# Kernel tuning notes

Measured on AMD Instinct MI355X. Metric: run time of the kernel, lower is better.

## Reference

```python
import jax, jax.numpy as jnp
import numpy as np

FEATURES = 1024
HEAD_DIM = 64
NUM_HEADS = 16
EPS = 1e-5


def setup_inputs() -> dict:
    key = jax.random.key(0)
    ks = jax.random.split(key, 6)
    x = jax.random.normal(ks[0], (2, 2048, FEATURES), dtype=jnp.float32)
    s_in = 1.0 / np.sqrt(FEATURES)
    s_hd = 1.0 / np.sqrt(NUM_HEADS * HEAD_DIM)
    return {
        "x": x,
        "gamma": jnp.ones((FEATURES,), jnp.float32),
        "beta": jnp.zeros((FEATURES,), jnp.float32),
        "Wq": jax.random.normal(ks[1], (FEATURES, NUM_HEADS * HEAD_DIM), jnp.float32) * s_in,
        "Wkv": jax.random.normal(ks[2], (FEATURES, 2 * HEAD_DIM), jnp.float32) * s_in,
        "Wo": jax.random.normal(ks[3], (NUM_HEADS * HEAD_DIM, FEATURES), jnp.float32) * s_hd,
        "bo": jax.random.normal(ks[4], (FEATURES,), jnp.float32) * s_hd,
    }


def reference(x, gamma, beta, Wq, Wkv, Wo, bo):
    # LayerNorm over last dim
    mu = jnp.mean(x, axis=-1, keepdims=True)
    var = jnp.mean(jnp.square(x - mu), axis=-1, keepdims=True)
    xn = (x - mu) * jax.lax.rsqrt(var + EPS) * gamma + beta

    b, t, _ = x.shape
    q = (xn @ Wq).reshape(b, t, NUM_HEADS, HEAD_DIM).transpose(0, 2, 1, 3)  # b h t d
    kv = xn @ Wkv  # b s 2d
    k, v = kv[..., :HEAD_DIM], kv[..., HEAD_DIM:]  # b s d (single shared head)

    scale = HEAD_DIM ** (-0.5)
    attn = jnp.einsum('bhtd,bsd->bhts', q, k) * scale
    attn = jax.nn.softmax(attn, axis=-1)
    out = jnp.einsum('bhts,bsd->bhtd', attn, v)
    out = out.transpose(0, 2, 1, 3).reshape(b, t, NUM_HEADS * HEAD_DIM)
    return out @ Wo + bo + x
```

## Files before the change

kernel.cpp:

```cpp
#include <hip/hip_runtime.h>

typedef __attribute__((ext_vector_type(8))) __bf16 bf16x8;
typedef __attribute__((ext_vector_type(4))) float floatx4;
typedef unsigned short u16;
typedef unsigned int u32;

#define KSCALE 0.18033688011112042f

__device__ __forceinline__ u16 f2bf(float f) {
    union { float f; u32 u; } v; v.f = f;
    u32 r = v.u + 0x7fffu + ((v.u >> 16) & 1u);
    return (u16)(r >> 16);
}

__device__ __forceinline__ u32 pk2bf(float a, float b) {
    union { float f; u32 u; } x, y; x.f = a; y.f = b;
    return __builtin_amdgcn_perm(y.u + 0x8000u, x.u + 0x8000u, 0x07060302);
}

__device__ __forceinline__ void gl_lds16(const u16* g, u16* l) {
    __builtin_amdgcn_global_load_lds((const __attribute__((address_space(1))) void*)g,
                                     (__attribute__((address_space(3))) void*)l, 16, 0, 0);
}

__global__ __launch_bounds__(256) void prep(const float* __restrict__ Wq, const float* __restrict__ Wkv,
                                            const float* __restrict__ Wo, const float* __restrict__ x,
                                            const float* __restrict__ gamma, const float* __restrict__ beta,
                                            u16* __restrict__ WqkvT, u16* __restrict__ WoT,
                                            u16* __restrict__ xn) {
    __shared__ float tile[64][68];
    __shared__ float ps[4], ps2[4];
    const int bx = blockIdx.x;
    const int t = threadIdx.x;
    if (bx < 768) {
        const int z = bx >> 8, rem = bx & 255;
        const int tr = (rem >> 4) * 64, tc = (rem & 15) * 64;
        const float* in = (z == 0) ? Wq : (z == 1 ? Wkv : Wo);
        u16* out = (z == 0) ? WqkvT : (z == 1 ? WqkvT + (size_t)1024 * 1024 : WoT);
        const int cols = (z == 1) ? 128 : 1024;
        if (tc >= cols) return;
        for (int p = 0; p < 4; p++) {
            int ri = (t >> 4) + p * 16;
            int ci = (t & 15) * 4;
            float4 v = *(const float4*)&in[(size_t)(tr + ri) * cols + tc + ci];
            tile[ri][ci + 0] = v.x; tile[ri][ci + 1] = v.y;
            tile[ri][ci + 2] = v.z; tile[ri][ci + 3] = v.w;
        }
        __syncthreads();
        for (int p = 0; p < 4; p++) {
            int oc = (t >> 4) + p * 16;
            int ir = (t & 15) * 4;
            float s = (z == 1 && (tc + oc) < 64) ? KSCALE : 1.0f;
            ushort4 o;
            o.x = f2bf(tile[ir + 0][oc] * s);
            o.y = f2bf(tile[ir + 1][oc] * s);
            o.z = f2bf(tile[ir + 2][oc] * s);
            o.w = f2bf(tile[ir + 3][oc] * s);
            *(ushort4*)&out[(size_t)(tc + oc) * 1024 + tr + ir] = o;
        }
    } else {
        const int row = bx - 768;
        const float* xr = x + (size_t)row * 1024;
        float4 v = *(const float4*)&xr[t * 4];
        float s = v.x + v.y + v.z + v.w;
        float s2 = v.x * v.x + v.y * v.y + v.z * v.z + v.w * v.w;
        for (int off = 1; off < 64; off <<= 1) {
            s += __shfl_xor(s, off, 64);
            s2 += __shfl_xor(s2, off, 64);
        }
        int w = t >> 6, lane = t & 63;
        if (lane == 0) { ps[w] = s; ps2[w] = s2; }
        __syncthreads();
        float S = ps[0] + ps[1] + ps[2] + ps[3];
        float S2 = ps2[0] + ps2[1] + ps2[2] + ps2[3];
        float mu = S * (1.0f / 1024.0f);
        float var = S2 * (1.0f / 1024.0f) - mu * mu;
        float rstd = rsqrtf(var + 1e-5f);
        ushort4 o;
        o.x = f2bf((v.x - mu) * rstd * gamma[t * 4 + 0] + beta[t * 4 + 0]);
        o.y = f2bf((v.y - mu) * rstd * gamma[t * 4 + 1] + beta[t * 4 + 1]);
        o.z = f2bf((v.z - mu) * rstd * gamma[t * 4 + 2] + beta[t * 4 + 2]);
        o.w = f2bf((v.w - mu) * rstd * gamma[t * 4 + 3] + beta[t * 4 + 3]);
        *(ushort4*)&xn[(size_t)row * 1024 + t * 4] = o;
    }
}

template <bool FINAL>
__global__ __launch_bounds__(256) void gemm_bt(const u16* __restrict__ A, const u16* __restrict__ BT,
                                               u16* __restrict__ Cb, float* __restrict__ Cf,
                                               const float* __restrict__ bias, const float* __restrict__ resid,
                                               u16* __restrict__ vt2, int M, int N, int K) {
    __shared__ u16 as_[2 * 64 * 64];
    __shared__ u16 bs_[2 * 128 * 64];
    const int t = threadIdx.x;
    const int w = t >> 6, lane = t & 63, q = lane >> 4, c = lane & 15;
    const int tm = blockIdx.y * 64, tn = blockIdx.x * 128;
    const int wm = (w & 1) * 32, wn = (w >> 1) * 64;

    const int l3 = lane >> 3, sch = lane & 7;
    const int arow = w * 16 + l3;
    const int aswz = (sch ^ (arow & 7)) * 8;
    const int brow = w * 32 + l3;
    const int bswz = (sch ^ (brow & 7)) * 8;
    const u16* ag0 = A + (size_t)(tm + arow) * K + aswz;
    const u16* ag1 = ag0 + (size_t)8 * K;
    const u16* bg0 = BT + (size_t)(tn + brow) * K + bswz;
    const u16* bg1 = bg0 + (size_t)8 * K;
    const u16* bg2 = bg0 + (size_t)16 * K;
    const u16* bg3 = bg0 + (size_t)24 * K;
    u16* al0 = as_ + (w * 16) * 64;
    u16* al1 = as_ + (w * 16 + 8) * 64;
    u16* bl0 = bs_ + (w * 32) * 64;
    u16* bl1 = bs_ + (w * 32 + 8) * 64;
    u16* bl2 = bs_ + (w * 32 + 16) * 64;
    u16* bl3 = bs_ + (w * 32 + 24) * 64;

    const int c7 = c & 7;
    const u16* afp[2][2];
    const u16* bfp[4][2];
#pragma unroll
    for (int i = 0; i < 2; i++)
#pragma unroll
        for (int kk = 0; kk < 2; kk++)
            afp[i][kk] = &as_[(wm + i * 16 + c) * 64 + (((kk * 4 + q) ^ c7) * 8)];
#pragma unroll
    for (int j = 0; j < 4; j++)
#pragma unroll
        for (int kk = 0; kk < 2; kk++)
            bfp[j][kk] = &bs_[(wn + j * 16 + c) * 64 + (((kk * 4 + q) ^ c7) * 8)];

    floatx4 acc[2][4];
    for (int i = 0; i < 2; i++)
        for (int j = 0; j < 4; j++) acc[i][j] = (floatx4){0.f, 0.f, 0.f, 0.f};

    gl_lds16(ag0, al0);
    gl_lds16(ag1, al1);
    gl_lds16(bg0, bl0);
    gl_lds16(bg1, bl1);
    gl_lds16(bg2, bl2);
    gl_lds16(bg3, bl3);
    __syncthreads();

    const int NIT = K >> 6;
#pragma unroll 2
    for (int it = 0; it < NIT; it++) {
        const int cur = it & 1, nxt = cur ^ 1;
        if (it + 1 < NIT) {
            const int k0 = (it + 1) << 6;
            gl_lds16(ag0 + k0, al0 + nxt * 4096);
            gl_lds16(ag1 + k0, al1 + nxt * 4096);
            gl_lds16(bg0 + k0, bl0 + nxt * 8192);
            gl_lds16(bg1 + k0, bl1 + nxt * 8192);
            gl_lds16(bg2 + k0, bl2 + nxt * 8192);
            gl_lds16(bg3 + k0, bl3 + nxt * 8192);
        }
        bf16x8 af[2][2], bf[4][2];
#pragma unroll
        for (int i = 0; i < 2; i++)
#pragma unroll
            for (int kk = 0; kk < 2; kk++)
                af[i][kk] = *(const bf16x8*)(afp[i][kk] + cur * 4096);
#pragma unroll
        for (int j = 0; j < 4; j++)
#pragma unroll
            for (int kk = 0; kk < 2; kk++)
                bf[j][kk] = *(const bf16x8*)(bfp[j][kk] + cur * 8192);
#pragma unroll
        for (int kk = 0; kk < 2; kk++)
#pragma unroll
            for (int i = 0; i < 2; i++)
#pragma unroll
                for (int j = 0; j < 4; j++)
                    acc[i][j] = __builtin_amdgcn_mfma_f32_16x16x32_bf16(af[i][kk], bf[j][kk], acc[i][j], 0, 0, 0);
        __syncthreads();
    }
#pragma unroll
    for (int i = 0; i < 2; i++)
#pragma unroll
        for (int j = 0; j < 4; j++)
#pragma unroll
            for (int r = 0; r < 4; r++) {
                int row = tm + wm + i * 16 + q * 4 + r;
                int col = tn + wn + j * 16 + c;
                float v = acc[i][j][r];
                if (FINAL) {
                    Cf[(size_t)row * N + col] = v + bias[col] + resid[(size_t)row * N + col];
                } else if (col < 1088) {
                    Cb[(size_t)row * N + col] = f2bf(v);
                } else {
                    int d = col - 1088;
                    int bb = row >> 11, sl = row & 2047;
                    int Bk = sl >> 5, u = sl & 31;
                    int up = ((u >> 2) & 3) * 8 + ((u >> 4) << 2) + (u & 3);
                    vt2[((size_t)(bb * 64 + d)) * 2048 + Bk * 32 + up] = f2bf(v);
                }
            }
}

union Vf { bf16x8 v; u32 w[4]; };

__global__ __launch_bounds__(256, 2) void attn9(const u16* __restrict__ qkv, const u16* __restrict__ vt2,
                                                u16* __restrict__ out) {
    __shared__ u16 ksm[2][64 * 64];
    __shared__ u16 vsm[2][64 * 64];
    const int t = threadIdx.x;
    const int w = t >> 6, lane = t & 63;
    const int q = lane >> 4, c = lane & 15;
    const int qt = blockIdx.x, hg = blockIdx.y, b = blockIdx.z;
    const int h = hg * 4 + w;
    const size_t qrow0 = (size_t)b * 2048 + qt * 32;
    const u16* kbase = qkv + (size_t)b * 2048 * 1152 + 1024;
    const u16* vbase = vt2 + (size_t)b * 64 * 2048;

    const int l3 = lane >> 3, sch = lane & 7;
    const int srow = w * 16 + l3;
    const int swz = (sch ^ (srow & 7)) * 8;
    const u16* kg0 = kbase + (size_t)srow * 1152 + swz;
    const u16* kg1 = kg0 + (size_t)8 * 1152;
    const u16* vg0 = vbase + (size_t)srow * 2048 + swz;
    const u16* vg1 = vg0 + (size_t)8 * 2048;
    u16* kl0 = &ksm[0][(w * 16) * 64];
    u16* kl1 = &ksm[0][(w * 16 + 8) * 64];
    u16* vl0 = &vsm[0][(w * 16) * 64];
    u16* vl1 = &vsm[0][(w * 16 + 8) * 64];

    const int c7 = c & 7;
    const u16* kfp[4][2];
    const u16* vfp[4][2];
#pragma unroll
    for (int ni = 0; ni < 4; ni++)
#pragma unroll
        for (int kk = 0; kk < 2; kk++) {
            kfp[ni][kk] = &ksm[0][(ni * 16 + c) * 64 + (((kk * 4 + q) ^ c7) * 8)];
            vfp[ni][kk] = &vsm[0][(ni * 16 + c) * 64 + (((kk * 4 + q) ^ c7) * 8)];
        }

    bf16x8 qf[2][2];
#pragma unroll
    for (int mi = 0; mi < 2; mi++)
#pragma unroll
        for (int kk = 0; kk < 2; kk++)
            qf[mi][kk] = *(const bf16x8*)&qkv[(qrow0 + mi * 16 + c) * 1152 + h * 64 + kk * 32 + q * 8];

    floatx4 O[4][2], Lacc[2];
#pragma unroll
    for (int di = 0; di < 4; di++)
#pragma unroll
        for (int mi = 0; mi < 2; mi++) O[di][mi] = (floatx4){0.f, 0.f, 0.f, 0.f};
    Lacc[0] = (floatx4){0.f, 0.f, 0.f, 0.f};
    Lacc[1] = (floatx4){0.f, 0.f, 0.f, 0.f};
    Vf ones;
    ones.w[0] = ones.w[1] = ones.w[2] = ones.w[3] = 0x3F803F80u;

    gl_lds16(kg0, kl0);
    gl_lds16(kg1, kl1);
    gl_lds16(vg0, vl0);
    gl_lds16(vg1, vl1);
    kg0 += (size_t)64 * 1152; kg1 += (size_t)64 * 1152; vg0 += 64; vg1 += 64;
    __syncthreads();

#pragma unroll 2
    for (int tt = 0; tt < 32; tt++) {
        const int cur = tt & 1, nxt = cur ^ 1;
        if (tt < 31) {
            gl_lds16(kg0, kl0 + nxt * 4096);
            gl_lds16(kg1, kl1 + nxt * 4096);
            gl_lds16(vg0, vl0 + nxt * 4096);
            gl_lds16(vg1, vl1 + nxt * 4096);
            kg0 += (size_t)64 * 1152; kg1 += (size_t)64 * 1152; vg0 += 64; vg1 += 64;
        }

        bf16x8 kf[4][2];
        Vf vf[4][2];
#pragma unroll
        for (int ni = 0; ni < 4; ni++)
#pragma unroll
            for (int kk = 0; kk < 2; kk++)
                kf[ni][kk] = *(const bf16x8*)(kfp[ni][kk] + cur * 4096);
#pragma unroll
        for (int di = 0; di < 4; di++)
#pragma unroll
            for (int kk = 0; kk < 2; kk++)
                vf[di][kk].v = *(const bf16x8*)(vfp[di][kk] + cur * 4096);

        floatx4 sacc[4][2];
#pragma unroll
        for (int ni = 0; ni < 4; ni++)
#pragma unroll
            for (int mi = 0; mi < 2; mi++) {
                floatx4 z = (floatx4){0.f, 0.f, 0.f, 0.f};
                z = __builtin_amdgcn_mfma_f32_16x16x32_bf16(kf[ni][0], qf[mi][0], z, 0, 0, 0);
                z = __builtin_amdgcn_mfma_f32_16x16x32_bf16(kf[ni][1], qf[mi][1], z, 0, 0, 0);
                sacc[ni][mi] = z;
            }

        u32 pk[4][2][2];
#pragma unroll
        for (int mi = 0; mi < 2; mi++)
#pragma unroll
            for (int ni = 0; ni < 4; ni++) {
                float p0 = __builtin_amdgcn_exp2f(sacc[ni][mi][0]);
                float p1 = __builtin_amdgcn_exp2f(sacc[ni][mi][1]);
                float p2 = __builtin_amdgcn_exp2f(sacc[ni][mi][2]);
                float p3 = __builtin_amdgcn_exp2f(sacc[ni][mi][3]);
                pk[ni][mi][0] = pk2bf(p0, p1);
                pk[ni][mi][1] = pk2bf(p2, p3);
            }

#pragma unroll
        for (int kk = 0; kk < 2; kk++) {
            Vf pf[2];
#pragma unroll
            for (int mi = 0; mi < 2; mi++) {
                pf[mi].w[0] = pk[2 * kk][mi][0];
                pf[mi].w[1] = pk[2 * kk][mi][1];
                pf[mi].w[2] = pk[2 * kk + 1][mi][0];
                pf[mi].w[3] = pk[2 * kk + 1][mi][1];
            }
#pragma unroll
            for (int di = 0; di < 4; di++)
#pragma unroll
                for (int mi = 0; mi < 2; mi++)
                    O[di][mi] = __builtin_amdgcn_mfma_f32_16x16x32_bf16(vf[di][kk].v, pf[mi].v, O[di][mi], 0, 0, 0);
#pragma unroll
            for (int mi = 0; mi < 2; mi++)
                Lacc[mi] = __builtin_amdgcn_mfma_f32_16x16x32_bf16(ones.v, pf[mi].v, Lacc[mi], 0, 0, 0);
        }

        __syncthreads();
    }

    float inv[2] = {1.0f / Lacc[0][0], 1.0f / Lacc[1][0]};
#pragma unroll
    for (int di = 0; di < 4; di++)
#pragma unroll
        for (int mi = 0; mi < 2; mi++) {
            ushort4 o;
            o.x = f2bf(O[di][mi][0] * inv[mi]);
            o.y = f2bf(O[di][mi][1] * inv[mi]);
            o.z = f2bf(O[di][mi][2] * inv[mi]);
            o.w = f2bf(O[di][mi][3] * inv[mi]);
            *(ushort4*)&out[(qrow0 + mi * 16 + c) * 1024 + h * 64 + di * 16 + q * 4] = o;
        }
}

extern "C" void kernel_launch(void* const* d_in, const int* in_sizes, int n_in,
                              void* d_out, int out_size, void* d_ws, size_t ws_size,
                              hipStream_t stream) {
    const float* x = (const float*)d_in[0];
    const float* gamma = (const float*)d_in[1];
    const float* beta = (const float*)d_in[2];
    const float* Wq = (const float*)d_in[3];
    const float* Wkv = (const float*)d_in[4];
    const float* Wo = (const float*)d_in[5];
    const float* bo = (const float*)d_in[6];
    float* out = (float*)d_out;

    u16* WqkvT = (u16*)d_ws;
    u16* WoT = WqkvT + (size_t)1152 * 1024;
    u16* xn = WoT + (size_t)1024 * 1024;
    u16* qkv = xn + (size_t)4096 * 1024;
    u16* vt2 = qkv + (size_t)4096 * 1152;
    u16* attnO = xn;

    prep<<<4864, 256, 0, stream>>>(Wq, Wkv, Wo, x, gamma, beta, WqkvT, WoT, xn);
    gemm_bt<false><<<dim3(9, 64), 256, 0, stream>>>(xn, WqkvT, qkv, nullptr, nullptr, nullptr, vt2,
                                                    4096, 1152, 1024);
    attn9<<<dim3(64, 4, 2), 256, 0, stream>>>(qkv, vt2, attnO);
    gemm_bt<true><<<dim3(8, 64), 256, 0, stream>>>(attnO, WoT, nullptr, out, bo, x, nullptr,
                                                   4096, 1024, 1024);
}
```

Measured before the change: 165.4 us.

## Merge all four stages into one cooperative persistent kernel with grid syncs

Replaces the four separate launches (prep, QKV GEMM, attention, output GEMM) with a single cooperative kernel of 512 blocks that loops over work units and separates the stages with grid-wide syncs. The prep stage also stops launching the idle Wkv tiles that previously returned early. The aim is to cut per-launch overhead and the drain and fill gaps between kernels. In exchange it fixes occupancy at two blocks per CU, gives the GEMM stages a persistent schedule that may balance poorly (576 tiles over 512 blocks), and adds the cost of the grid syncs. If the cooperative launch fails it falls back to the separate kernels.

Result: slower. 511.9 us (+209.5%).

```diff
diff --git a/kernel.cpp b/kernel.cpp
--- a/kernel.cpp
+++ b/kernel.cpp
@@ -1,4 +1,6 @@
 #include <hip/hip_runtime.h>
+#include <hip/hip_cooperative_groups.h>
+namespace cg = cooperative_groups;
 
 typedef __attribute__((ext_vector_type(8))) __bf16 bf16x8;
 typedef __attribute__((ext_vector_type(4))) float floatx4;
@@ -23,22 +25,20 @@
                                      (__attribute__((address_space(3))) void*)l, 16, 0, 0);
 }
 
-__global__ __launch_bounds__(256) void prep(const float* __restrict__ Wq, const float* __restrict__ Wkv,
-                                            const float* __restrict__ Wo, const float* __restrict__ x,
-                                            const float* __restrict__ gamma, const float* __restrict__ beta,
-                                            u16* __restrict__ WqkvT, u16* __restrict__ WoT,
-                                            u16* __restrict__ xn) {
-    __shared__ float tile[64][68];
-    __shared__ float ps[4], ps2[4];
-    const int bx = blockIdx.x;
-    const int t = threadIdx.x;
-    if (bx < 768) {
-        const int z = bx >> 8, rem = bx & 255;
-        const int tr = (rem >> 4) * 64, tc = (rem & 15) * 64;
-        const float* in = (z == 0) ? Wq : (z == 1 ? Wkv : Wo);
-        u16* out = (z == 0) ? WqkvT : (z == 1 ? WqkvT + (size_t)1024 * 1024 : WoT);
-        const int cols = (z == 1) ? 128 : 1024;
-        if (tc >= cols) return;
+__device__ __forceinline__ void prep_unit(unsigned char* smb, int t, int u,
+                                          const float* __restrict__ Wq, const float* __restrict__ Wkv,
+                                          const float* __restrict__ Wo, const float* __restrict__ x,
+                                          const float* __restrict__ gamma, const float* __restrict__ beta,
+                                          u16* __restrict__ WqkvT, u16* __restrict__ WoT,
+                                          u16* __restrict__ xn) {
+    float (*tile)[68] = (float(*)[68])smb;
+    float* ps = (float*)(smb + 17408);
+    float* ps2 = ps + 4;
+    if (u < 544) {
+        const float* in; u16* outw; int cols, tr, tc;
+        if (u < 256) { in = Wq; outw = WqkvT; cols = 1024; tr = (u >> 4) * 64; tc = (u & 15) * 64; }
+        else if (u < 288) { int r = u - 256; in = Wkv; outw = WqkvT + (size_t)1024 * 1024; cols = 128; tr = (r >> 1) * 64; tc = (r & 1) * 64; }
+        else { int r = u - 288; in = Wo; outw = WoT; cols = 1024; tr = (r >> 4) * 64; tc = (r & 15) * 64; }
         for (int p = 0; p < 4; p++) {
             int ri = (t >> 4) + p * 16;
             int ci = (t & 15) * 4;
@@ -47,19 +47,20 @@
             tile[ri][ci + 2] = v.z; tile[ri][ci + 3] = v.w;
         }
         __syncthreads();
+        const bool kcol = (cols == 128);
         for (int p = 0; p < 4; p++) {
             int oc = (t >> 4) + p * 16;
             int ir = (t & 15) * 4;
-            float s = (z == 1 && (tc + oc) < 64) ? KSCALE : 1.0f;
+            float s = (kcol && (tc + oc) < 64) ? KSCALE : 1.0f;
             ushort4 o;
             o.x = f2bf(tile[ir + 0][oc] * s);
             o.y = f2bf(tile[ir + 1][oc] * s);
             o.z = f2bf(tile[ir + 2][oc] * s);
             o.w = f2bf(tile[ir + 3][oc] * s);
-            *(ushort4*)&out[(size_t)(tc + oc) * 1024 + tr + ir] = o;
+            *(ushort4*)&outw[(size_t)(tc + oc) * 1024 + tr + ir] = o;
         }
     } else {
-        const int row = bx - 768;
+        const int row = u - 544;
         const float* xr = x + (size_t)row * 1024;
         float4 v = *(const float4*)&xr[t * 4];
         float s = v.x + v.y + v.z + v.w;
@@ -86,15 +87,14 @@
 }
 
 template <bool FINAL>
-__global__ __launch_bounds__(256) void gemm_bt(const u16* __restrict__ A, const u16* __restrict__ BT,
-                                               u16* __restrict__ Cb, float* __restrict__ Cf,
-                                               const float* __restrict__ bias, const float* __restrict__ resid,
-                                               u16* __restrict__ vt2, int M, int N, int K) {
-    __shared__ u16 as_[2 * 64 * 64];
-    __shared__ u16 bs_[2 * 128 * 64];
-    const int t = threadIdx.x;
+__device__ __forceinline__ void gemm_unit(u16* smem, int t, int tm, int tn,
+                                          const u16* __restrict__ A, const u16* __restrict__ BT,
+                                          u16* __restrict__ Cb, float* __restrict__ Cf,
+                                          const float* __restrict__ bias, const float* __restrict__ resid,
+                                          u16* __restrict__ vt2, int N, int K) {
+    u16* as_ = smem;
+    u16* bs_ = smem + 8192;
     const int w = t >> 6, lane = t & 63, q = lane >> 4, c = lane & 15;
-    const int tm = blockIdx.y * 64, tn = blockIdx.x * 128;
     const int wm = (w & 1) * 32, wn = (w >> 1) * 64;
 
     const int l3 = lane >> 3, sch = lane & 7;
@@ -122,15 +122,17 @@
     for (int i = 0; i < 2; i++)
 #pragma unroll
         for (int kk = 0; kk < 2; kk++)
-            afp[i][kk] = &as_[(wm + i * 16 + c) * 64 + (((kk * 4 + q) ^ c7) * 8)];
+            afp[i][kk] = as_ + (wm + i * 16 + c) * 64 + (((kk * 4 + q) ^ c7) * 8);
 #pragma unroll
     for (int j = 0; j < 4; j++)
 #pragma unroll
         for (int kk = 0; kk < 2; kk++)
-            bfp[j][kk] = &bs_[(wn + j * 16 + c) * 64 + (((kk * 4 + q) ^ c7) * 8)];
+            bfp[j][kk] = bs_ + (wn + j * 16 + c) * 64 + (((kk * 4 + q) ^ c7) * 8);
 
     floatx4 acc[2][4];
+#pragma unroll
     for (int i = 0; i < 2; i++)
+#pragma unroll
         for (int j = 0; j < 4; j++) acc[i][j] = (floatx4){0.f, 0.f, 0.f, 0.f};
 
     gl_lds16(ag0, al0);
@@ -190,8 +192,8 @@
                 } else {
                     int d = col - 1088;
                     int bb = row >> 11, sl = row & 2047;
-                    int Bk = sl >> 5, u = sl & 31;
-                    int up = ((u >> 2) & 3) * 8 + ((u >> 4) << 2) + (u & 3);
+                    int Bk = sl >> 5, uu = sl & 31;
+                    int up = ((uu >> 2) & 3) * 8 + ((uu >> 4) << 2) + (uu & 3);
                     vt2[((size_t)(bb * 64 + d)) * 2048 + Bk * 32 + up] = f2bf(v);
                 }
             }
@@ -199,14 +201,13 @@
 
 union Vf { bf16x8 v; u32 w[4]; };
 
-__global__ __launch_bounds__(256, 2) void attn9(const u16* __restrict__ qkv, const u16* __restrict__ vt2,
-                                                u16* __restrict__ out) {
-    __shared__ u16 ksm[2][64 * 64];
-    __shared__ u16 vsm[2][64 * 64];
-    const int t = threadIdx.x;
+__device__ __forceinline__ void attn_unit(u16* smem, int t, int qt, int hg, int b,
+                                          const u16* __restrict__ qkv, const u16* __restrict__ vt2,
+                                          u16* __restrict__ out) {
+    u16* ksm = smem;
+    u16* vsm = smem + 8192;
     const int w = t >> 6, lane = t & 63;
     const int q = lane >> 4, c = lane & 15;
-    const int qt = blockIdx.x, hg = blockIdx.y, b = blockIdx.z;
     const int h = hg * 4 + w;
     const size_t qrow0 = (size_t)b * 2048 + qt * 32;
     const u16* kbase = qkv + (size_t)b * 2048 * 1152 + 1024;
@@ -219,10 +220,10 @@
     const u16* kg1 = kg0 + (size_t)8 * 1152;
     const u16* vg0 = vbase + (size_t)srow * 2048 + swz;
     const u16* vg1 = vg0 + (size_t)8 * 2048;
-    u16* kl0 = &ksm[0][(w * 16) * 64];
-    u16* kl1 = &ksm[0][(w * 16 + 8) * 64];
-    u16* vl0 = &vsm[0][(w * 16) * 64];
-    u16* vl1 = &vsm[0][(w * 16 + 8) * 64];
+    u16* kl0 = ksm + (w * 16) * 64;
+    u16* kl1 = ksm + (w * 16 + 8) * 64;
+    u16* vl0 = vsm + (w * 16) * 64;
+    u16* vl1 = vsm + (w * 16 + 8) * 64;
 
     const int c7 = c & 7;
     const u16* kfp[4][2];
@@ -231,8 +232,8 @@
     for (int ni = 0; ni < 4; ni++)
 #pragma unroll
         for (int kk = 0; kk < 2; kk++) {
-            kfp[ni][kk] = &ksm[0][(ni * 16 + c) * 64 + (((kk * 4 + q) ^ c7) * 8)];
-            vfp[ni][kk] = &vsm[0][(ni * 16 + c) * 64 + (((kk * 4 + q) ^ c7) * 8)];
+            kfp[ni][kk] = ksm + (ni * 16 + c) * 64 + (((kk * 4 + q) ^ c7) * 8);
+            vfp[ni][kk] = vsm + (ni * 16 + c) * 64 + (((kk * 4 + q) ^ c7) * 8);
         }
 
     bf16x8 qf[2][2];
@@ -344,29 +345,91 @@
         }
 }
 
+__global__ __launch_bounds__(256, 2) void mega(const float* __restrict__ Wq, const float* __restrict__ Wkv,
+                                               const float* __restrict__ Wo, const float* __restrict__ x,
+                                               const float* __restrict__ gamma, const float* __restrict__ beta,
+                                               const float* __restrict__ bo, u16* __restrict__ WqkvT,
+                                               u16* __restrict__ WoT, u16* __restrict__ xn,
+                                               u16* __restrict__ qkv, u16* __restrict__ vt2,
+                                               float* __restrict__ out) {
+    __shared__ __align__(16) u16 smem[24576];
+    cg::grid_group grid = cg::this_grid();
+    const int bid = blockIdx.x, t = threadIdx.x;
+
+    for (int u = bid; u < 4640; u += 512) {
+        prep_unit((unsigned char*)smem, t, u, Wq, Wkv, Wo, x, gamma, beta, WqkvT, WoT, xn);
+        __syncthreads();
+    }
+    __threadfence();
+    grid.sync();
+
+    for (int u = bid; u < 576; u += 512)
+        gemm_unit<false>(smem, t, (u / 9) * 64, (u % 9) * 128, xn, WqkvT, qkv, nullptr, nullptr, nullptr,
+                         vt2, 1152, 1024);
+    __threadfence();
+    grid.sync();
+
+    attn_unit(smem, t, bid & 63, (bid >> 6) & 3, bid >> 8, qkv, vt2, xn);
+    __threadfence();
+    grid.sync();
+
+    gemm_unit<true>(smem, t, (bid >> 3) * 64, (bid & 7) * 128, xn, WoT, nullptr, out, bo, x, nullptr,
+                    1024, 1024);
+}
+
+__global__ __launch_bounds__(256) void prep_k(const float* __restrict__ Wq, const float* __restrict__ Wkv,
+                                              const float* __restrict__ Wo, const float* __restrict__ x,
+                                              const float* __restrict__ gamma, const float* __restrict__ beta,
+                                              u16* __restrict__ WqkvT, u16* __restrict__ WoT,
+                                              u16* __restrict__ xn) {
+    __shared__ __align__(16) unsigned char smb[17440];
+    prep_unit(smb, threadIdx.x, blockIdx.x, Wq, Wkv, Wo, x, gamma, beta, WqkvT, WoT, xn);
+}
+
+template <bool FINAL>
+__global__ __launch_bounds__(256) void gemm_k(const u16* __restrict__ A, const u16* __restrict__ BT,
+                                              u16* __restrict__ Cb, float* __restrict__ Cf,
+                                              const float* __restrict__ bias, const float* __restrict__ resid,
+                                              u16* __restrict__ vt2, int N, int K) {
+    __shared__ __align__(16) u16 smem[24576];
+    gemm_unit<FINAL>(smem, threadIdx.x, blockIdx.y * 64, blockIdx.x * 128, A, BT, Cb, Cf, bias, resid,
+                     vt2, N, K);
+}
+
+__global__ __launch_bounds__(256, 2) void attn_k(const u16* __restrict__ qkv, const u16* __restrict__ vt2,
+                                                 u16* __restrict__ out) {
+    __shared__ __align__(16) u16 smem[16384];
+    attn_unit(smem, threadIdx.x, blockIdx.x, blockIdx.y, blockIdx.z, qkv, vt2, out);
+}
+
 extern "C" void kernel_launch(void* const* d_in, const int* in_sizes, int n_in,
                               void* d_out, int out_size, void* d_ws, size_t ws_size,
                               hipStream_t stream) {
-    const float* x = (const float*)d_in[0];
-    const float* gamma = (const float*)d_in[1];
-    const float* beta = (const float*)d_in[2];
-    const float* Wq = (const float*)d_in[3];
-    const float* Wkv = (const float*)d_in[4];
-    const float* Wo = (const float*)d_in[5];
-    const float* bo = (const float*)d_in[6];
-    float* out = (float*)d_out;
+    const float* Wq_x = (const float*)d_in[3];
+    const float* Wkv_x = (const float*)d_in[4];
+    const float* Wo_x = (const float*)d_in[5];
+    const float* x_x = (const float*)d_in[0];
+    const float* gamma_x = (const float*)d_in[1];
+    const float* beta_x = (const float*)d_in[2];
+    const float* bo_x = (const float*)d_in[6];
+    float* out_x = (float*)d_out;
 
     u16* WqkvT = (u16*)d_ws;
     u16* WoT = WqkvT + (size_t)1152 * 1024;
     u16* xn = WoT + (size_t)1024 * 1024;
     u16* qkv = xn + (size_t)4096 * 1024;
     u16* vt2 = qkv + (size_t)4096 * 1152;
-    u16* attnO = xn;
-
-    prep<<<4864, 256, 0, stream>>>(Wq, Wkv, Wo, x, gamma, beta, WqkvT, WoT, xn);
-    gemm_bt<false><<<dim3(9, 64), 256, 0, stream>>>(xn, WqkvT, qkv, nullptr, nullptr, nullptr, vt2,
-                                                    4096, 1152, 1024);
-    attn9<<<dim3(64, 4, 2), 256, 0, stream>>>(qkv, vt2, attnO);
-    gemm_bt<true><<<dim3(8, 64), 256, 0, stream>>>(attnO, WoT, nullptr, out, bo, x, nullptr,
-                                                   4096, 1024, 1024);
-}
+
+    void* kargs[13] = {(void*)&Wq_x, (void*)&Wkv_x, (void*)&Wo_x, (void*)&x_x, (void*)&gamma_x,
+                       (void*)&beta_x, (void*)&bo_x, (void*)&WqkvT, (void*)&WoT, (void*)&xn,
+                       (void*)&qkv, (void*)&vt2, (void*)&out_x};
+    hipError_t err = hipLaunchCooperativeKernel((const void*)mega, dim3(512), dim3(256), kargs, 0, stream);
+    if (err != hipSuccess) {
+        prep_k<<<4640, 256, 0, stream>>>(Wq_x, Wkv_x, Wo_x, x_x, gamma_x, beta_x, WqkvT, WoT, xn);
+        gemm_k<false><<<dim3(9, 64), 256, 0, stream>>>(xn, WqkvT, qkv, nullptr, nullptr, nullptr, vt2,
+                                                       1152, 1024);
+        attn_k<<<dim3(64, 4, 2), 256, 0, stream>>>(qkv, vt2, xn);
+        gemm_k<true><<<dim3(8, 64), 256, 0, stream>>>(xn, WoT, nullptr, out_x, bo_x, x_x, nullptr,
+                                                      1024, 1024);
+    }
+}
```
